# Kernel optimization log

Measured on AMD Instinct MI355X. Metric: run time of the kernel, lower is better.

Reference implementation:

```python
import jax, jax.numpy as jnp
import numpy as np


def setup_inputs() -> dict:
    key = jax.random.key(0)
    k1, k2 = jax.random.split(key)
    B, H, L = 8, 768, 4096
    x = jax.random.normal(k1, (B, H, L), dtype=jnp.float32)
    k = jax.random.normal(k2, (H, L), dtype=jnp.float32)
    return {"x": x, "k": k, "n": L}


def reference(x, k, n):
    # FFT-based long convolution: fft(x) * fft(k), inverse fft, real part,
    # truncated to the input sequence length. Inputs are real, so rfft/irfft
    # compute the identical result to complex fft + .real, at half the work.
    L = x.shape[-1]
    xf = jnp.fft.rfft(x, n=n)                 # [B, H, n//2+1] complex
    kf = jnp.fft.rfft(k, n=n)                 # [H, n//2+1]   complex
    y = jnp.fft.irfft(xf * kf, n=n)[..., :L]  # [B, H, L]
    return y.astype(x.dtype)
```

## Files before the change

### kernel.cpp

```cpp
#include <hip/hip_runtime.h>
#include <math.h>


#define NT 256
#define KF_LD 2049
#define C_SQRT1_2 0.70710678118654752f
#define C_COS_PI8 0.92387953251128675f
#define C_SIN_PI8 0.38268343236508977f
#define INV_2048 4.8828125e-4f
#define INV_4096 2.44140625e-4f

#define SW(a) ((a) ^ (((a) >> 5) & 31) ^ (((a) >> 2) & 24))
__device__ __forceinline__ int WP(int a) {
  const int s = SW(a);
  return 2 * s - (s & 63);
}

__device__ __forceinline__ void sincos_rev(float f, float& sn, float& cs) {
  float s_, c_;
  asm("v_sin_f32 %0, %1" : "=v"(s_) : "v"(f));
  asm("v_cos_f32 %0, %1" : "=v"(c_) : "v"(f));
  sn = s_; cs = c_;
}

template <int SIGN>
__device__ __forceinline__ void bf8(const float ar[8], const float ai[8],
                                    float br[8], float bi[8]) {
  float s0r = ar[0] + ar[4], s0i = ai[0] + ai[4];
  float s1r = ar[0] - ar[4], s1i = ai[0] - ai[4];
  float s2r = ar[2] + ar[6], s2i = ai[2] + ai[6];
  float s3r = ar[2] - ar[6], s3i = ai[2] - ai[6];
  float E0r = s0r + s2r, E0i = s0i + s2i;
  float E2r = s0r - s2r, E2i = s0i - s2i;
  float E1r, E1i, E3r, E3i;
  if (SIGN < 0) { E1r = s1r + s3i; E1i = s1i - s3r; E3r = s1r - s3i; E3i = s1i + s3r; }
  else          { E1r = s1r - s3i; E1i = s1i + s3r; E3r = s1r + s3i; E3i = s1i - s3r; }
  float u0r = ar[1] + ar[5], u0i = ai[1] + ai[5];
  float u1r = ar[1] - ar[5], u1i = ai[1] - ai[5];
  float u2r = ar[3] + ar[7], u2i = ai[3] + ai[7];
  float u3r = ar[3] - ar[7], u3i = ai[3] - ai[7];
  float O0r = u0r + u2r, O0i = u0i + u2i;
  float O2r = u0r - u2r, O2i = u0i - u2i;
  float O1r, O1i, O3r, O3i;
  if (SIGN < 0) { O1r = u1r + u3i; O1i = u1i - u3r; O3r = u1r - u3i; O3i = u1i + u3r; }
  else          { O1r = u1r - u3i; O1i = u1i + u3r; O3r = u1r + u3i; O3i = u1i - u3r; }
  float t1r, t1i, t2r, t2i, t3r, t3i;
  if (SIGN < 0) {
    t1r = C_SQRT1_2 * (O1r + O1i); t1i = C_SQRT1_2 * (O1i - O1r);
    t2r = O2i;  t2i = -O2r;
    t3r = C_SQRT1_2 * (O3i - O3r); t3i = -C_SQRT1_2 * (O3r + O3i);
  } else {
    t1r = C_SQRT1_2 * (O1r - O1i); t1i = C_SQRT1_2 * (O1i + O1r);
    t2r = -O2i; t2i = O2r;
    t3r = -C_SQRT1_2 * (O3r + O3i); t3i = C_SQRT1_2 * (O3r - O3i);
  }
  br[0] = E0r + O0r; bi[0] = E0i + O0i;
  br[4] = E0r - O0r; bi[4] = E0i - O0i;
  br[1] = E1r + t1r; bi[1] = E1i + t1i;
  br[5] = E1r - t1r; bi[5] = E1i - t1i;
  br[2] = E2r + t2r; bi[2] = E2i + t2i;
  br[6] = E2r - t2r; bi[6] = E2i - t2i;
  br[3] = E3r + t3r; bi[3] = E3i + t3i;
  br[7] = E3r - t3r; bi[7] = E3i - t3i;
}

template <int SIGN, int S>
__device__ __forceinline__ void tw_write(float* Y, int ob,
                                         const float br[8], const float bi[8],
                                         float f1) {
  { const int i0 = WP(ob); Y[i0] = br[0]; Y[i0 + 64] = bi[0]; }
  float sn, cs;
  sincos_rev(f1, sn, cs);
  const float w1r = cs, w1i = (SIGN > 0) ? sn : -sn;
  float cwr = w1r, cwi = w1i;
#pragma unroll
  for (int m = 1; m < 8; ++m) {
    const int idx = WP(ob + S * m);
    Y[idx] = br[m] * cwr - bi[m] * cwi;
    Y[idx + 64] = br[m] * cwi + bi[m] * cwr;
    if (m < 7) {
      const float nr = cwr * w1r - cwi * w1i;
      const float ni = cwr * w1i + cwi * w1r;
      cwr = nr; cwi = ni;
    }
  }
}

template <int SIGN, int S>
__device__ __forceinline__ void stage_r8(const float* X, float* Y,
                                         const int rd[8]) {
  const int t = (int)threadIdx.x;
  const int q = t & (S - 1);
  const int p = t / S;
  float ar[8], ai[8];
#pragma unroll
  for (int j = 0; j < 8; ++j) {
    ar[j] = X[rd[j]];
    ai[j] = X[rd[j] + 64];
  }
  float br[8], bi[8];
  bf8<SIGN>(ar, ai, br, bi);
  tw_write<SIGN, S>(Y, q + 8 * S * p, br, bi, (float)(S * p) * INV_2048);
}

template <int SIGN>
__device__ __forceinline__ void stage1_global(const float2* __restrict__ src,
                                              float* Y) {
  const int t = (int)threadIdx.x;
  float ar[8], ai[8];
#pragma unroll
  for (int j = 0; j < 8; ++j) {
    const float2 v = src[t + 256 * j];
    ar[j] = v.x; ai[j] = v.y;
  }
  float br[8], bi[8];
  bf8<SIGN>(ar, ai, br, bi);
  tw_write<SIGN, 1>(Y, 8 * t, br, bi, (float)t * INV_2048);
}

__device__ __forceinline__ void bf4f(const float* X, int b,
                                     float orr[4], float oi[4]) {
  const int i0 = WP(b), i1 = WP(b + 512), i2 = WP(b + 1024), i3 = WP(b + 1536);
  float a0r = X[i0], a0i = X[i0 + 64];
  float a1r = X[i1], a1i = X[i1 + 64];
  float a2r = X[i2], a2i = X[i2 + 64];
  float a3r = X[i3], a3i = X[i3 + 64];
  float s0r = a0r + a2r, s0i = a0i + a2i;
  float s1r = a0r - a2r, s1i = a0i - a2i;
  float s2r = a1r + a3r, s2i = a1i + a3i;
  float s3r = a1r - a3r, s3i = a1i - a3i;
  orr[0] = s0r + s2r; oi[0] = s0i + s2i;
  orr[1] = s1r + s3i; oi[1] = s1i - s3r;
  orr[2] = s0r - s2r; oi[2] = s0i - s2i;
  orr[3] = s1r - s3i; oi[3] = s1i + s3r;
}

__device__ __forceinline__ void pw_pair(int klo, float Pr, float Pi, float Qr,
                                        float Qi, const float2* __restrict__ kfrow,
                                        float cs, float sn,
                                        float2& zlo, float2& zhi) {
  const float Er = 0.5f * (Pr + Qr), Ei = 0.5f * (Pi - Qi);
  const float Or = 0.5f * (Pi + Qi), Oi = 0.5f * (Qr - Pr);
  const float Xpr = Er + cs * Or + sn * Oi, Xpi = Ei + cs * Oi - sn * Or;
  const float Xqr = Er - cs * Or - sn * Oi, Xqi = -Ei + cs * Oi - sn * Or;
  const float2 Kp = kfrow[klo];
  const float2 Kq = kfrow[2048 - klo];
  const float Ypr = Xpr * Kp.x - Xpi * Kp.y, Ypi = Xpr * Kp.y + Xpi * Kp.x;
  const float Yqr = Xqr * Kq.x - Xqi * Kq.y, Yqi = Xqr * Kq.y + Xqi * Kq.x;
  const float Epr = 0.5f * (Ypr + Yqr), Epi = 0.5f * (Ypi - Yqi);
  const float Dr = 0.5f * (Ypr - Yqr), Di = 0.5f * (Ypi + Yqi);
  zlo = make_float2(Epr - cs * Di - sn * Dr, Epi + cs * Dr - sn * Di);
  zhi = make_float2(Epr + cs * Di + sn * Dr, -Epi + cs * Dr - sn * Di);
}

__device__ __forceinline__ void fwd4_pw(const float* X, float* Y,
                                        const float2* __restrict__ kfrow) {
  const int t = (int)threadIdx.x;
  const int b1 = (t == 0) ? 256 : 512 - t;
  float Ar[4], Ai[4], Br[4], Bi[4];
  bf4f(X, t, Ar, Ai);
  bf4f(X, b1, Br, Bi);
  int k0, k1, k2, k3;
  float2 zl0, zh0, zl1, zh1, zl2, zh2, zl3, zh3, zl4;
  zl4 = make_float2(0.f, 0.f);
  if (t == 0) {
    float2 zh4;
    k0 = 0;   pw_pair(0,   Ar[0], Ai[0], Ar[0], Ai[0], kfrow, 1.0f, 0.0f, zl0, zh0);
    k1 = 512; pw_pair(512, Ar[1], Ai[1], Ar[3], Ai[3], kfrow, C_SQRT1_2, C_SQRT1_2, zl1, zh1);
    k2 = 256; pw_pair(256, Br[0], Bi[0], Br[3], Bi[3], kfrow, C_COS_PI8, C_SIN_PI8, zl2, zh2);
    k3 = 768; pw_pair(768, Br[1], Bi[1], Br[2], Bi[2], kfrow, C_SIN_PI8, C_COS_PI8, zl3, zh3);
    pw_pair(1024, Ar[2], Ai[2], Ar[2], Ai[2], kfrow, 0.0f, 1.0f, zl4, zh4);
  } else {
    float s, c;
    sincos_rev((float)t * INV_4096, s, c);
    const float pr = C_SQRT1_2 * (c - s);
    const float ps = C_SQRT1_2 * (c + s);
    k0 = t;        pw_pair(k0, Ar[0], Ai[0], Br[3], Bi[3], kfrow, c, s, zl0, zh0);
    k1 = t + 512;  pw_pair(k1, Ar[1], Ai[1], Br[2], Bi[2], kfrow, pr, ps, zl1, zh1);
    k2 = 1024 - t; pw_pair(k2, Br[1], Bi[1], Ar[2], Ai[2], kfrow, s, c, zl2, zh2);
    k3 = 512 - t;  pw_pair(k3, Br[0], Bi[0], Ar[3], Ai[3], kfrow, ps, pr, zl3, zh3);
  }
  {
    int i;
    i = WP(k0);                 Y[i] = zl0.x; Y[i + 64] = zl0.y;
    i = WP((2048 - k0) & 2047); Y[i] = zh0.x; Y[i + 64] = zh0.y;
    i = WP(k1);                 Y[i] = zl1.x; Y[i + 64] = zl1.y;
    i = WP(2048 - k1);          Y[i] = zh1.x; Y[i + 64] = zh1.y;
    i = WP(k2);                 Y[i] = zl2.x; Y[i + 64] = zl2.y;
    i = WP(2048 - k2);          Y[i] = zh2.x; Y[i + 64] = zh2.y;
    i = WP(k3);                 Y[i] = zl3.x; Y[i + 64] = zl3.y;
    i = WP(2048 - k3);          Y[i] = zh3.x; Y[i + 64] = zh3.y;
    if (t == 0) { i = WP(1024); Y[i] = zl4.x; Y[i + 64] = zl4.y; }
  }
}

__device__ __forceinline__ void inv4_store(const float* X,
                                           float2* __restrict__ dst) {
  const int t = (int)threadIdx.x;
#pragma unroll
  for (int c = 0; c < 2; ++c) {
    const int b = t + 256 * c;
    const int i0 = WP(b), i1 = WP(b + 512), i2 = WP(b + 1024), i3 = WP(b + 1536);
    float a0r = X[i0], a0i = X[i0 + 64];
    float a1r = X[i1], a1i = X[i1 + 64];
    float a2r = X[i2], a2i = X[i2 + 64];
    float a3r = X[i3], a3i = X[i3 + 64];
    float s0r = a0r + a2r, s0i = a0i + a2i;
    float s1r = a0r - a2r, s1i = a0i - a2i;
    float s2r = a1r + a3r, s2i = a1i + a3i;
    float s3r = a1r - a3r, s3i = a1i - a3i;
    dst[b]        = make_float2(s0r + s2r, s0i + s2i);
    dst[b + 512]  = make_float2(s1r - s3i, s1i + s3r);
    dst[b + 1024] = make_float2(s0r - s2r, s0i - s2i);
    dst[b + 1536] = make_float2(s1r + s3i, s1i - s3r);
  }
}

__device__ __forceinline__ void stage_r4_fwd(const float* X, float* Y) {
  const int t = (int)threadIdx.x;
  float O0r[4], O0i[4], O1r[4], O1i[4];
  bf4f(X, t, O0r, O0i);
  bf4f(X, t + 256, O1r, O1i);
#pragma unroll
  for (int m = 0; m < 4; ++m) {
    int i;
    i = WP(t + 512 * m);       Y[i] = O0r[m]; Y[i + 64] = O0i[m];
    i = WP(t + 256 + 512 * m); Y[i] = O1r[m]; Y[i + 64] = O1i[m];
  }
}

__device__ __forceinline__ void unpackX(float Pr, float Pi, float Qr, float Qi,
                                        int kk, float2& Xp, float2& Xq) {
  const float Er = 0.5f * (Pr + Qr), Ei = 0.5f * (Pi - Qi);
  const float Or = 0.5f * (Pi + Qi), Oi = 0.5f * (Qr - Pr);
  float sn, cs;
  sincos_rev((float)kk * INV_4096, sn, cs);
  Xp = make_float2(Er + cs * Or + sn * Oi, Ei + cs * Oi - sn * Or);
  Xq = make_float2(Er - cs * Or - sn * Oi, -Ei + cs * Oi - sn * Or);
}

__global__ __launch_bounds__(NT) void kfft_kernel(const float* __restrict__ kin,
                                                  float2* __restrict__ kf) {
  __shared__ float A_[4096];
  __shared__ float B_[4096];
  const int t = (int)threadIdx.x;
  const int h = (int)blockIdx.x;
  const float2* src = (const float2*)(kin + (size_t)h * 4096);
  int rd[8];
#pragma unroll
  for (int j = 0; j < 8; ++j) rd[j] = WP(t + 256 * j);
  stage1_global<-1>(src, A_);
  __syncthreads();
  stage_r8<-1, 8>(A_, B_, rd);
  __syncthreads();
  stage_r8<-1, 64>(B_, A_, rd);
  __syncthreads();
  stage_r4_fwd(A_, B_);
  __syncthreads();
  const float sc = 1.0f / 2048.0f;
  float2* kfrow = kf + (size_t)h * KF_LD;
#pragma unroll
  for (int u = 0; u < 4; ++u) {
    const int kk = t + 256 * u;
    const int ip = WP(kk), iq = WP((2048 - kk) & 2047);
    float2 Xp, Xq;
    unpackX(B_[ip], B_[ip + 64], B_[iq], B_[iq + 64], kk, Xp, Xq);
    kfrow[kk] = make_float2(Xp.x * sc, Xp.y * sc);
    kfrow[2048 - kk] = make_float2(Xq.x * sc, Xq.y * sc);
  }
  if (t == 0) {
    const int ip = WP(1024);
    float2 Xp, Xq;
    unpackX(B_[ip], B_[ip + 64], B_[ip], B_[ip + 64], 1024, Xp, Xq);
    kfrow[1024] = make_float2(Xp.x * sc, Xp.y * sc);
  }
}

__global__ __launch_bounds__(NT) void conv_kernel(const float* __restrict__ x,
                                                  const float2* __restrict__ kf,
                                                  float* __restrict__ y, int H) {
  __shared__ float A_[4096];
  __shared__ float B_[4096];
  const int row = (int)blockIdx.x;
  const int h = row % H;
  const float2* src = (const float2*)(x + (size_t)row * 4096);
  float2* dst = (float2*)(y + (size_t)row * 4096);
  const float2* kfrow = kf + (size_t)h * KF_LD;
  const int t = (int)threadIdx.x;
  int rd[8];
#pragma unroll
  for (int j = 0; j < 8; ++j) rd[j] = WP(t + 256 * j);
  stage1_global<-1>(src, A_);
  __syncthreads();
  stage_r8<-1, 8>(A_, B_, rd);
  __syncthreads();
  stage_r8<-1, 64>(B_, A_, rd);
  __syncthreads();
  fwd4_pw(A_, B_, kfrow);
  __syncthreads();
  stage_r8<1, 1>(B_, A_, rd);
  __syncthreads();
  stage_r8<1, 8>(A_, B_, rd);
  __syncthreads();
  stage_r8<1, 64>(B_, A_, rd);
  __syncthreads();
  inv4_store(A_, dst);
}

extern "C" void kernel_launch(void* const* d_in, const int* in_sizes, int n_in,
                              void* d_out, int out_size, void* d_ws, size_t ws_size,
                              hipStream_t stream) {
  const float* x = (const float*)d_in[0];
  const float* kin = (const float*)d_in[1];
  float* y = (float*)d_out;
  const int H = in_sizes[1] / 4096;
  const int BH = in_sizes[0] / 4096;
  float2* kf = (float2*)d_ws;
  hipLaunchKernelGGL(kfft_kernel, dim3(H), dim3(NT), 0, stream, kin, kf);
  hipLaunchKernelGGL(conv_kernel, dim3(BH), dim3(NT), 0, stream, x, kf, y, H);
}
```

Baseline: 65.85 us.

## Pack two real rows into one complex 4096-point FFT per block

```diff
diff --git a/kernel.cpp b/kernel.cpp
--- a/kernel.cpp
+++ b/kernel.cpp
@@ -2,12 +2,9 @@
 #include <math.h>
 
 
-#define NT 256
+#define NT 512
 #define KF_LD 2049
 #define C_SQRT1_2 0.70710678118654752f
-#define C_COS_PI8 0.92387953251128675f
-#define C_SIN_PI8 0.38268343236508977f
-#define INV_2048 4.8828125e-4f
 #define INV_4096 2.44140625e-4f
 
 #define SW(a) ((a) ^ (((a) >> 5) & 31) ^ (((a) >> 2) & 24))
@@ -100,203 +97,152 @@
   }
   float br[8], bi[8];
   bf8<SIGN>(ar, ai, br, bi);
-  tw_write<SIGN, S>(Y, q + 8 * S * p, br, bi, (float)(S * p) * INV_2048);
-}
-
-template <int SIGN>
-__device__ __forceinline__ void stage1_global(const float2* __restrict__ src,
-                                              float* Y) {
-  const int t = (int)threadIdx.x;
-  float ar[8], ai[8];
-#pragma unroll
-  for (int j = 0; j < 8; ++j) {
-    const float2 v = src[t + 256 * j];
-    ar[j] = v.x; ai[j] = v.y;
-  }
-  float br[8], bi[8];
-  bf8<SIGN>(ar, ai, br, bi);
-  tw_write<SIGN, 1>(Y, 8 * t, br, bi, (float)t * INV_2048);
-}
-
-__device__ __forceinline__ void bf4f(const float* X, int b,
-                                     float orr[4], float oi[4]) {
-  const int i0 = WP(b), i1 = WP(b + 512), i2 = WP(b + 1024), i3 = WP(b + 1536);
-  float a0r = X[i0], a0i = X[i0 + 64];
-  float a1r = X[i1], a1i = X[i1 + 64];
-  float a2r = X[i2], a2i = X[i2 + 64];
-  float a3r = X[i3], a3i = X[i3 + 64];
-  float s0r = a0r + a2r, s0i = a0i + a2i;
-  float s1r = a0r - a2r, s1i = a0i - a2i;
-  float s2r = a1r + a3r, s2i = a1i + a3i;
-  float s3r = a1r - a3r, s3i = a1i - a3i;
-  orr[0] = s0r + s2r; oi[0] = s0i + s2i;
-  orr[1] = s1r + s3i; oi[1] = s1i - s3r;
-  orr[2] = s0r - s2r; oi[2] = s0i - s2i;
-  orr[3] = s1r - s3i; oi[3] = s1i + s3r;
-}
-
-__device__ __forceinline__ void pw_pair(int klo, float Pr, float Pi, float Qr,
-                                        float Qi, const float2* __restrict__ kfrow,
-                                        float cs, float sn,
-                                        float2& zlo, float2& zhi) {
-  const float Er = 0.5f * (Pr + Qr), Ei = 0.5f * (Pi - Qi);
-  const float Or = 0.5f * (Pi + Qi), Oi = 0.5f * (Qr - Pr);
-  const float Xpr = Er + cs * Or + sn * Oi, Xpi = Ei + cs * Oi - sn * Or;
-  const float Xqr = Er - cs * Or - sn * Oi, Xqi = -Ei + cs * Oi - sn * Or;
-  const float2 Kp = kfrow[klo];
-  const float2 Kq = kfrow[2048 - klo];
-  const float Ypr = Xpr * Kp.x - Xpi * Kp.y, Ypi = Xpr * Kp.y + Xpi * Kp.x;
-  const float Yqr = Xqr * Kq.x - Xqi * Kq.y, Yqi = Xqr * Kq.y + Xqi * Kq.x;
-  const float Epr = 0.5f * (Ypr + Yqr), Epi = 0.5f * (Ypi - Yqi);
-  const float Dr = 0.5f * (Ypr - Yqr), Di = 0.5f * (Ypi + Yqi);
-  zlo = make_float2(Epr - cs * Di - sn * Dr, Epi + cs * Dr - sn * Di);
-  zhi = make_float2(Epr + cs * Di + sn * Dr, -Epi + cs * Dr - sn * Di);
-}
-
-__device__ __forceinline__ void fwd4_pw(const float* X, float* Y,
-                                        const float2* __restrict__ kfrow) {
-  const int t = (int)threadIdx.x;
-  const int b1 = (t == 0) ? 256 : 512 - t;
-  float Ar[4], Ai[4], Br[4], Bi[4];
-  bf4f(X, t, Ar, Ai);
-  bf4f(X, b1, Br, Bi);
-  int k0, k1, k2, k3;
-  float2 zl0, zh0, zl1, zh1, zl2, zh2, zl3, zh3, zl4;
-  zl4 = make_float2(0.f, 0.f);
-  if (t == 0) {
-    float2 zh4;
-    k0 = 0;   pw_pair(0,   Ar[0], Ai[0], Ar[0], Ai[0], kfrow, 1.0f, 0.0f, zl0, zh0);
-    k1 = 512; pw_pair(512, Ar[1], Ai[1], Ar[3], Ai[3], kfrow, C_SQRT1_2, C_SQRT1_2, zl1, zh1);
-    k2 = 256; pw_pair(256, Br[0], Bi[0], Br[3], Bi[3], kfrow, C_COS_PI8, C_SIN_PI8, zl2, zh2);
-    k3 = 768; pw_pair(768, Br[1], Bi[1], Br[2], Bi[2], kfrow, C_SIN_PI8, C_COS_PI8, zl3, zh3);
-    pw_pair(1024, Ar[2], Ai[2], Ar[2], Ai[2], kfrow, 0.0f, 1.0f, zl4, zh4);
-  } else {
-    float s, c;
-    sincos_rev((float)t * INV_4096, s, c);
-    const float pr = C_SQRT1_2 * (c - s);
-    const float ps = C_SQRT1_2 * (c + s);
-    k0 = t;        pw_pair(k0, Ar[0], Ai[0], Br[3], Bi[3], kfrow, c, s, zl0, zh0);
-    k1 = t + 512;  pw_pair(k1, Ar[1], Ai[1], Br[2], Bi[2], kfrow, pr, ps, zl1, zh1);
-    k2 = 1024 - t; pw_pair(k2, Br[1], Bi[1], Ar[2], Ai[2], kfrow, s, c, zl2, zh2);
-    k3 = 512 - t;  pw_pair(k3, Br[0], Bi[0], Ar[3], Ai[3], kfrow, ps, pr, zl3, zh3);
-  }
-  {
-    int i;
-    i = WP(k0);                 Y[i] = zl0.x; Y[i + 64] = zl0.y;
-    i = WP((2048 - k0) & 2047); Y[i] = zh0.x; Y[i + 64] = zh0.y;
-    i = WP(k1);                 Y[i] = zl1.x; Y[i + 64] = zl1.y;
-    i = WP(2048 - k1);          Y[i] = zh1.x; Y[i + 64] = zh1.y;
-    i = WP(k2);                 Y[i] = zl2.x; Y[i + 64] = zl2.y;
-    i = WP(2048 - k2);          Y[i] = zh2.x; Y[i + 64] = zh2.y;
-    i = WP(k3);                 Y[i] = zl3.x; Y[i + 64] = zl3.y;
-    i = WP(2048 - k3);          Y[i] = zh3.x; Y[i + 64] = zh3.y;
-    if (t == 0) { i = WP(1024); Y[i] = zl4.x; Y[i + 64] = zl4.y; }
-  }
-}
-
-__device__ __forceinline__ void inv4_store(const float* X,
-                                           float2* __restrict__ dst) {
-  const int t = (int)threadIdx.x;
-#pragma unroll
-  for (int c = 0; c < 2; ++c) {
-    const int b = t + 256 * c;
-    const int i0 = WP(b), i1 = WP(b + 512), i2 = WP(b + 1024), i3 = WP(b + 1536);
-    float a0r = X[i0], a0i = X[i0 + 64];
-    float a1r = X[i1], a1i = X[i1 + 64];
-    float a2r = X[i2], a2i = X[i2 + 64];
-    float a3r = X[i3], a3i = X[i3 + 64];
-    float s0r = a0r + a2r, s0i = a0i + a2i;
-    float s1r = a0r - a2r, s1i = a0i - a2i;
-    float s2r = a1r + a3r, s2i = a1i + a3i;
-    float s3r = a1r - a3r, s3i = a1i - a3i;
-    dst[b]        = make_float2(s0r + s2r, s0i + s2i);
-    dst[b + 512]  = make_float2(s1r - s3i, s1i + s3r);
-    dst[b + 1024] = make_float2(s0r - s2r, s0i - s2i);
-    dst[b + 1536] = make_float2(s1r + s3i, s1i - s3r);
-  }
-}
-
-__device__ __forceinline__ void stage_r4_fwd(const float* X, float* Y) {
-  const int t = (int)threadIdx.x;
-  float O0r[4], O0i[4], O1r[4], O1i[4];
-  bf4f(X, t, O0r, O0i);
-  bf4f(X, t + 256, O1r, O1i);
+  tw_write<SIGN, S>(Y, q + 8 * S * p, br, bi, (float)(S * p) * INV_4096);
+}
+
+__device__ __forceinline__ void stage1_conv(const float* __restrict__ x0,
+                                            const float* __restrict__ x1,
+                                            float* Y) {
+  const int t = (int)threadIdx.x;
+  float ar[8], ai[8];
+#pragma unroll
+  for (int j = 0; j < 8; ++j) {
+    ar[j] = x0[t + 512 * j];
+    ai[j] = x1[t + 512 * j];
+  }
+  float br[8], bi[8];
+  bf8<-1>(ar, ai, br, bi);
+  tw_write<-1, 1>(Y, 8 * t, br, bi, (float)t * INV_4096);
+}
+
+__device__ __forceinline__ void stage4_kf(const float* X, float* Y,
+                                          const float2* __restrict__ kfrow,
+                                          const int rd[8]) {
+  const int t = (int)threadIdx.x;
+  float ar[8], ai[8];
+#pragma unroll
+  for (int j = 0; j < 8; ++j) {
+    ar[j] = X[rd[j]];
+    ai[j] = X[rd[j] + 64];
+  }
+  float br[8], bi[8];
+  bf8<-1>(ar, ai, br, bi);
+#pragma unroll
+  for (int m = 0; m < 8; ++m) {
+    const int k = t + 512 * m;
+    float2 kv;
+    if (m <= 3) {
+      kv = kfrow[k];
+    } else {
+      kv = kfrow[4096 - k];
+      kv.y = -kv.y;
+    }
+    const int i = WP(k);
+    Y[i] = br[m] * kv.x - bi[m] * kv.y;
+    Y[i + 64] = br[m] * kv.y + bi[m] * kv.x;
+  }
+}
+
+__device__ __forceinline__ void stage4_store(const float* X,
+                                             float* __restrict__ y0,
+                                             float* __restrict__ y1,
+                                             const int rd[8]) {
+  const int t = (int)threadIdx.x;
+  float ar[8], ai[8];
+#pragma unroll
+  for (int j = 0; j < 8; ++j) {
+    ar[j] = X[rd[j]];
+    ai[j] = X[rd[j] + 64];
+  }
+  float br[8], bi[8];
+  bf8<1>(ar, ai, br, bi);
+#pragma unroll
+  for (int m = 0; m < 8; ++m) {
+    const int k = t + 512 * m;
+    y0[k] = br[m];
+    y1[k] = bi[m];
+  }
+}
+
+__device__ __forceinline__ void stage1_k(const float* __restrict__ kin,
+                                         float* Y) {
+  const int t = (int)threadIdx.x;
+  float ar[8], ai[8];
+#pragma unroll
+  for (int j = 0; j < 8; ++j) {
+    ar[j] = kin[t + 512 * j];
+    ai[j] = 0.0f;
+  }
+  float br[8], bi[8];
+  bf8<-1>(ar, ai, br, bi);
+  tw_write<-1, 1>(Y, 8 * t, br, bi, (float)t * INV_4096);
+}
+
+__device__ __forceinline__ void stage4_kstore(const float* X,
+                                              float2* __restrict__ kfrow,
+                                              const int rd[8]) {
+  const int t = (int)threadIdx.x;
+  float ar[8], ai[8];
+#pragma unroll
+  for (int j = 0; j < 8; ++j) {
+    ar[j] = X[rd[j]];
+    ai[j] = X[rd[j] + 64];
+  }
+  float br[8], bi[8];
+  bf8<-1>(ar, ai, br, bi);
+  const float sc = 1.0f / 4096.0f;
 #pragma unroll
   for (int m = 0; m < 4; ++m) {
-    int i;
-    i = WP(t + 512 * m);       Y[i] = O0r[m]; Y[i + 64] = O0i[m];
-    i = WP(t + 256 + 512 * m); Y[i] = O1r[m]; Y[i + 64] = O1i[m];
-  }
-}
-
-__device__ __forceinline__ void unpackX(float Pr, float Pi, float Qr, float Qi,
-                                        int kk, float2& Xp, float2& Xq) {
-  const float Er = 0.5f * (Pr + Qr), Ei = 0.5f * (Pi - Qi);
-  const float Or = 0.5f * (Pi + Qi), Oi = 0.5f * (Qr - Pr);
-  float sn, cs;
-  sincos_rev((float)kk * INV_4096, sn, cs);
-  Xp = make_float2(Er + cs * Or + sn * Oi, Ei + cs * Oi - sn * Or);
-  Xq = make_float2(Er - cs * Or - sn * Oi, -Ei + cs * Oi - sn * Or);
+    const int k = t + 512 * m;
+    kfrow[k] = make_float2(br[m] * sc, bi[m] * sc);
+  }
+  if (t == 0) kfrow[2048] = make_float2(br[4] * sc, bi[4] * sc);
 }
 
 __global__ __launch_bounds__(NT) void kfft_kernel(const float* __restrict__ kin,
                                                   float2* __restrict__ kf) {
-  __shared__ float A_[4096];
-  __shared__ float B_[4096];
+  __shared__ float A_[8192];
+  __shared__ float B_[8192];
   const int t = (int)threadIdx.x;
   const int h = (int)blockIdx.x;
-  const float2* src = (const float2*)(kin + (size_t)h * 4096);
   int rd[8];
 #pragma unroll
-  for (int j = 0; j < 8; ++j) rd[j] = WP(t + 256 * j);
-  stage1_global<-1>(src, A_);
+  for (int j = 0; j < 8; ++j) rd[j] = WP(t + 512 * j);
+  stage1_k(kin + (size_t)h * 4096, A_);
   __syncthreads();
   stage_r8<-1, 8>(A_, B_, rd);
   __syncthreads();
   stage_r8<-1, 64>(B_, A_, rd);
   __syncthreads();
-  stage_r4_fwd(A_, B_);
-  __syncthreads();
-  const float sc = 1.0f / 2048.0f;
-  float2* kfrow = kf + (size_t)h * KF_LD;
-#pragma unroll
-  for (int u = 0; u < 4; ++u) {
-    const int kk = t + 256 * u;
-    const int ip = WP(kk), iq = WP((2048 - kk) & 2047);
-    float2 Xp, Xq;
-    unpackX(B_[ip], B_[ip + 64], B_[iq], B_[iq + 64], kk, Xp, Xq);
-    kfrow[kk] = make_float2(Xp.x * sc, Xp.y * sc);
-    kfrow[2048 - kk] = make_float2(Xq.x * sc, Xq.y * sc);
-  }
-  if (t == 0) {
-    const int ip = WP(1024);
-    float2 Xp, Xq;
-    unpackX(B_[ip], B_[ip + 64], B_[ip], B_[ip + 64], 1024, Xp, Xq);
-    kfrow[1024] = make_float2(Xp.x * sc, Xp.y * sc);
-  }
+  stage4_kstore(A_, kf + (size_t)h * KF_LD, rd);
 }
 
 __global__ __launch_bounds__(NT) void conv_kernel(const float* __restrict__ x,
                                                   const float2* __restrict__ kf,
                                                   float* __restrict__ y, int H) {
-  __shared__ float A_[4096];
-  __shared__ float B_[4096];
-  const int row = (int)blockIdx.x;
-  const int h = row % H;
-  const float2* src = (const float2*)(x + (size_t)row * 4096);
-  float2* dst = (float2*)(y + (size_t)row * 4096);
+  __shared__ float A_[8192];
+  __shared__ float B_[8192];
+  const int bi = (int)blockIdx.x;
+  const int h = bi % H;
+  const int j = bi / H;
+  const size_t r0 = (size_t)(2 * j) * H + h;
+  const size_t r1 = r0 + H;
+  const float* src0 = x + r0 * 4096;
+  const float* src1 = x + r1 * 4096;
+  float* dst0 = y + r0 * 4096;
+  float* dst1 = y + r1 * 4096;
   const float2* kfrow = kf + (size_t)h * KF_LD;
   const int t = (int)threadIdx.x;
   int rd[8];
 #pragma unroll
-  for (int j = 0; j < 8; ++j) rd[j] = WP(t + 256 * j);
-  stage1_global<-1>(src, A_);
+  for (int jj = 0; jj < 8; ++jj) rd[jj] = WP(t + 512 * jj);
+  stage1_conv(src0, src1, A_);
   __syncthreads();
   stage_r8<-1, 8>(A_, B_, rd);
   __syncthreads();
   stage_r8<-1, 64>(B_, A_, rd);
   __syncthreads();
-  fwd4_pw(A_, B_, kfrow);
+  stage4_kf(A_, B_, kfrow, rd);
   __syncthreads();
   stage_r8<1, 1>(B_, A_, rd);
   __syncthreads();
@@ -304,7 +250,7 @@
   __syncthreads();
   stage_r8<1, 64>(B_, A_, rd);
   __syncthreads();
-  inv4_store(A_, dst);
+  stage4_store(A_, dst0, dst1, rd);
 }
 
 extern "C" void kernel_launch(void* const* d_in, const int* in_sizes, int n_in,
@@ -317,5 +263,5 @@
   const int BH = in_sizes[0] / 4096;
   float2* kf = (float2*)d_ws;
   hipLaunchKernelGGL(kfft_kernel, dim3(H), dim3(NT), 0, stream, kin, kf);
-  hipLaunchKernelGGL(conv_kernel, dim3(BH), dim3(NT), 0, stream, x, kf, y, H);
-}
+  hipLaunchKernelGGL(conv_kernel, dim3(BH / 2), dim3(NT), 0, stream, x, kf, y, H);
+}
```

Result: faster. 62.74 us (-4.7%).
